# Performance work log

Hardware: AMD Instinct MI355X
Metric: run time of the kernel (lower is better)

Reference implementation:

```python
import jax, jax.numpy as jnp
import numpy as np

N = 100000   # nodes
E = 400000   # edges
P = 250000   # permutations (substructures)
L = 16       # lrp_length
D = 16       # lrp_out_dim
M = P * L    # perm-length rows of the sparse gather matrices


def setup_inputs() -> dict:
    key = jax.random.key(0)
    ks = jax.random.split(key, 16)
    return {
        "nfeat": jax.random.normal(ks[0], (N, D), dtype=jnp.float32),
        "efeat_idx": jax.random.randint(ks[1], (E,), 0, 4, dtype=jnp.int64),
        "n_row": jnp.arange(M, dtype=jnp.int64),
        "n_col": jax.random.randint(ks[2], (M,), 0, N, dtype=jnp.int64),
        "n_val": jax.random.uniform(ks[3], (M,), dtype=jnp.float32),
        "e_row": jnp.arange(M, dtype=jnp.int64),
        "e_col": jax.random.randint(ks[4], (M,), 0, E, dtype=jnp.int64),
        "e_val": jax.random.uniform(ks[5], (M,), dtype=jnp.float32),
        "p_row": jax.random.randint(ks[6], (P,), 0, N, dtype=jnp.int64),
        "p_col": jnp.arange(P, dtype=jnp.int64),
        "p_val": jax.random.uniform(ks[7], (P,), dtype=jnp.float32),
        "degs": jax.random.uniform(ks[8], (N,), dtype=jnp.float32) * 10.0,
        "weights": jax.random.normal(ks[9], (D, D, L), dtype=jnp.float32),
        "bias": jnp.zeros((1, D), dtype=jnp.float32),
        "W0": jax.random.normal(ks[10], (1, 2 * D), dtype=jnp.float32),
        "b0": jnp.zeros((2 * D,), dtype=jnp.float32),
        "W1": jax.random.normal(ks[11], (2 * D, D), dtype=jnp.float32),
        "b1": jnp.zeros((D,), dtype=jnp.float32),
        "bond_emb": jax.random.normal(ks[12], (4, D), dtype=jnp.float32),
    }


def _spmm(row, col, val, mat, m):
    # torch_sparse.spmm(index, value, m, n, mat): out[r] += val * mat[c]
    return jax.ops.segment_sum(val[:, None] * mat[col], row, num_segments=m)


def reference(nfeat, efeat_idx, n_row, n_col, n_val, e_row, e_col, e_val,
              p_row, p_col, p_val, degs, weights, bias, W0, b0, W1, b1, bond_emb):
    efeat = bond_emb[efeat_idx]                              # [E, D]
    x = _spmm(n_row, n_col, n_val, nfeat, M) \
        + _spmm(e_row, e_col, e_val, efeat, M)               # [M, D], M = P*L
    # transpose(0,1).view(D, -1, L).permute(1, 2, 0) -> [P, L, D]
    x = x.T.reshape(D, P, L).transpose(1, 2, 0)
    # einsum('dab,bca->dc'): d=P, a=L, b=D_in, c=D_out
    x = jax.nn.relu(jnp.einsum('pld,dcl->pc', x, weights) + bias)  # [P, D]
    pooled = _spmm(p_row, p_col, p_val, x, N)                # [N, D]
    # degree gate MLP: 1 -> 2D -> D
    fd = jax.nn.relu(degs[:, None] @ W0 + b0) @ W1 + b1      # [N, D]
    return pooled * fd
```

## Files before the change

kernel.cpp:

```cpp
#include <hip/hip_runtime.h>

#define NP 250000
#define NN 100000
#define NE 400000
#define LL 16
#define DD 16
#define MM (NP * LL)
#define NTILES (NP / 16)

typedef __bf16 bf16x8 __attribute__((ext_vector_type(8)));
typedef float f32x4 __attribute__((ext_vector_type(4)));

__device__ __forceinline__ float4 fma4(float a, float4 b, float4 c) {
    float4 r;
    r.x = fmaf(a, b.x, c.x);
    r.y = fmaf(a, b.y, c.y);
    r.z = fmaf(a, b.z, c.z);
    r.w = fmaf(a, b.w, c.w);
    return r;
}

__global__ __launch_bounds__(256) void init_kernel(
    const float* __restrict__ w,
    const float* __restrict__ nfeat,
    const float* __restrict__ bond_emb,
    const int* __restrict__ e_col,
    const int* __restrict__ efeat_idx,
    const float* __restrict__ degs,
    const float* __restrict__ W0,
    const float* __restrict__ b0,
    const float* __restrict__ W1,
    const float* __restrict__ b1,
    __bf16* __restrict__ wfrag,
    __bf16* __restrict__ nfeat_bf,
    __bf16* __restrict__ bond_bf,
    unsigned char* __restrict__ be2,
    float* __restrict__ fd,
    float* __restrict__ out)
{
    int t = blockIdx.x * 256 + threadIdx.x;
    if (t < 4096) {
        int kb = t >> 9;
        int lane = (t >> 3) & 63;
        int j = t & 7;
        int quad = lane >> 4, c = lane & 15;
        int d = ((quad & 1) << 3) + j;
        int l = ((quad >> 1) << 3) + kb;
        wfrag[t] = (__bf16)w[d * 256 + c * 16 + l];
    }
    if (t < NN * DD) {
        nfeat_bf[t] = (__bf16)nfeat[t];
        out[t] = 0.f;
    }
    if (t < 64) bond_bf[t] = (__bf16)bond_emb[t];
    if (t < MM / 4) {
        int4 ec = *(const int4*)(e_col + t * 4);
        unsigned int c0 = (unsigned int)efeat_idx[ec.x] & 3u;
        unsigned int c1 = (unsigned int)efeat_idx[ec.y] & 3u;
        unsigned int c2 = (unsigned int)efeat_idx[ec.z] & 3u;
        unsigned int c3 = (unsigned int)efeat_idx[ec.w] & 3u;
        be2[t] = (unsigned char)(c0 | (c1 << 2) | (c2 << 4) | (c3 << 6));
    }
    if (fd != nullptr && t < NN) {
        float dg = degs[t];
        float4 a0 = ((const float4*)b1)[0];
        float4 a1 = ((const float4*)b1)[1];
        float4 a2 = ((const float4*)b1)[2];
        float4 a3 = ((const float4*)b1)[3];
#pragma unroll
        for (int j2 = 0; j2 < 32; ++j2) {
            float h = fmaxf(fmaf(dg, W0[j2], b0[j2]), 0.f);
            const float4* w1r = (const float4*)(W1 + j2 * 16);
            a0 = fma4(h, w1r[0], a0);
            a1 = fma4(h, w1r[1], a1);
            a2 = fma4(h, w1r[2], a2);
            a3 = fma4(h, w1r[3], a3);
        }
        float4* o = (float4*)(fd + (size_t)t * DD);
        o[0] = a0; o[1] = a1; o[2] = a2; o[3] = a3;
    }
}

__global__ __launch_bounds__(256) void perm_kernel(
    const __bf16* __restrict__ nfeat_bf,
    const int* __restrict__ n_col,
    const float* __restrict__ n_val,
    const float* __restrict__ e_val,
    const unsigned char* __restrict__ be2,
    const int* __restrict__ p_row,
    const float* __restrict__ p_val,
    const __bf16* __restrict__ wfrag,
    const float* __restrict__ bias,
    const __bf16* __restrict__ bond_bf,
    const float* __restrict__ fd,
    float* __restrict__ out)
{
    const int wid = threadIdx.x >> 6;
    const int lane = threadIdx.x & 63;
    const int tile = blockIdx.x * 4 + wid;
    if (tile >= NTILES) return;
    const int quad = lane >> 4;
    const int col = lane & 15;
    const int half = quad & 1;
    const int lhalf = quad >> 1;

    const int pbase = tile * 16;
    const int mbase = (pbase + col) * LL + lhalf * 8;

    int4   nca = *(const int4*)(n_col + mbase);
    int4   ncb = *(const int4*)(n_col + mbase + 4);
    float4 nva = *(const float4*)(n_val + mbase);
    float4 nvb = *(const float4*)(n_val + mbase + 4);
    float4 eva = *(const float4*)(e_val + mbase);
    float4 evb = *(const float4*)(e_val + mbase + 4);
    unsigned int be16 = *(const unsigned short*)(be2 + (mbase >> 2));
    int4   pr  = *(const int4*)(p_row + pbase + quad * 4);
    float4 pvv = *(const float4*)(p_val + pbase + quad * 4);

    int   prs[4] = {pr.x, pr.y, pr.z, pr.w};
    float gv[4] = {1.f, 1.f, 1.f, 1.f};
    if (fd != nullptr) {
#pragma unroll
        for (int r = 0; r < 4; ++r)
            gv[r] = fd[(size_t)prs[r] * DD + col];
    }

    bf16x8 wf[8];
#pragma unroll
    for (int kb = 0; kb < 8; ++kb)
        wf[kb] = *(const bf16x8*)(wfrag + (kb * 64 + lane) * 8);
    const bf16x8 bq0 = *(const bf16x8*)(bond_bf + 0 * 16 + half * 8);
    const bf16x8 bq1 = *(const bf16x8*)(bond_bf + 1 * 16 + half * 8);
    const bf16x8 bq2 = *(const bf16x8*)(bond_bf + 2 * 16 + half * 8);
    const bf16x8 bq3 = *(const bf16x8*)(bond_bf + 3 * 16 + half * 8);
    const float bias_c = bias[col];

    int   ncs[8] = {nca.x, nca.y, nca.z, nca.w, ncb.x, ncb.y, ncb.z, ncb.w};
    float nvs[8] = {nva.x, nva.y, nva.z, nva.w, nvb.x, nvb.y, nvb.z, nvb.w};
    float evs[8] = {eva.x, eva.y, eva.z, eva.w, evb.x, evb.y, evb.z, evb.w};

    bf16x8 nfr[8];
#pragma unroll
    for (int kb = 0; kb < 8; ++kb)
        nfr[kb] = *(const bf16x8*)(nfeat_bf + ncs[kb] * DD + half * 8);

    f32x4 acc = {0.f, 0.f, 0.f, 0.f};
#pragma unroll
    for (int kb = 0; kb < 8; ++kb) {
        unsigned int b = (be16 >> (2 * kb)) & 3u;
        bf16x8 blo = (b & 1) ? bq1 : bq0;
        bf16x8 bhi = (b & 1) ? bq3 : bq2;
        bf16x8 bsel = (b & 2) ? bhi : blo;
        float nv = nvs[kb], ev = evs[kb];
        bf16x8 af;
#pragma unroll
        for (int j = 0; j < 8; ++j)
            af[j] = (__bf16)fmaf(nv, (float)nfr[kb][j], ev * (float)bsel[j]);
        acc = __builtin_amdgcn_mfma_f32_16x16x32_bf16(af, wf[kb], acc, 0, 0, 0);
    }

    float pvs[4] = {pvv.x, pvv.y, pvv.z, pvv.w};
#pragma unroll
    for (int r = 0; r < 4; ++r) {
        float v = fmaxf(acc[r] + bias_c, 0.f) * pvs[r] * gv[r];
        unsafeAtomicAdd(out + (size_t)prs[r] * DD + col, v);
    }
}

__global__ __launch_bounds__(256) void gate_kernel(
    const float* __restrict__ degs,
    const float* __restrict__ W0,
    const float* __restrict__ b0,
    const float* __restrict__ W1,
    const float* __restrict__ b1,
    float* __restrict__ out)
{
    int n = blockIdx.x * 256 + threadIdx.x;
    if (n >= NN) return;
    float dg = degs[n];
    float4 a0 = ((const float4*)b1)[0];
    float4 a1 = ((const float4*)b1)[1];
    float4 a2 = ((const float4*)b1)[2];
    float4 a3 = ((const float4*)b1)[3];
#pragma unroll
    for (int j = 0; j < 32; ++j) {
        float h = fmaxf(fmaf(dg, W0[j], b0[j]), 0.f);
        const float4* w1r = (const float4*)(W1 + j * 16);
        a0 = fma4(h, w1r[0], a0);
        a1 = fma4(h, w1r[1], a1);
        a2 = fma4(h, w1r[2], a2);
        a3 = fma4(h, w1r[3], a3);
    }
    float4* o = (float4*)(out + (size_t)n * DD);
    float4 v0 = o[0], v1 = o[1], v2 = o[2], v3 = o[3];
    v0.x *= a0.x; v0.y *= a0.y; v0.z *= a0.z; v0.w *= a0.w;
    v1.x *= a1.x; v1.y *= a1.y; v1.z *= a1.z; v1.w *= a1.w;
    v2.x *= a2.x; v2.y *= a2.y; v2.z *= a2.z; v2.w *= a2.w;
    v3.x *= a3.x; v3.y *= a3.y; v3.z *= a3.z; v3.w *= a3.w;
    o[0] = v0; o[1] = v1; o[2] = v2; o[3] = v3;
}

extern "C" void kernel_launch(void* const* d_in, const int* in_sizes, int n_in,
                              void* d_out, int out_size, void* d_ws, size_t ws_size,
                              hipStream_t stream) {
    const float* nfeat     = (const float*)d_in[0];
    const int*   efeat_idx = (const int*)d_in[1];
    const int*   n_col     = (const int*)d_in[3];
    const float* n_val     = (const float*)d_in[4];
    const int*   e_col     = (const int*)d_in[6];
    const float* e_val     = (const float*)d_in[7];
    const int*   p_row     = (const int*)d_in[8];
    const float* p_val     = (const float*)d_in[10];
    const float* degs      = (const float*)d_in[11];
    const float* weights   = (const float*)d_in[12];
    const float* bias      = (const float*)d_in[13];
    const float* W0        = (const float*)d_in[14];
    const float* b0        = (const float*)d_in[15];
    const float* W1        = (const float*)d_in[16];
    const float* b1        = (const float*)d_in[17];
    const float* bond_emb  = (const float*)d_in[18];

    float* out = (float*)d_out;

    char* wsb = (char*)d_ws;
    __bf16*        wfrag    = (__bf16*)wsb;
    __bf16*        nfeat_bf = (__bf16*)(wsb + 8192);
    __bf16*        bond_bf  = (__bf16*)(wsb + 8192 + 3200000);
    unsigned char* be2      = (unsigned char*)(wsb + 8192 + 3200000 + 128);
    const size_t base_need  = 8192 + 3200000 + 128 + 1000000;
    const bool   fuse_gate  = ws_size >= base_need + (size_t)NN * DD * 4;
    float*         fd       = fuse_gate ? (float*)(wsb + base_need) : nullptr;

    init_kernel<<<(NN * DD + 255) / 256, 256, 0, stream>>>(
        weights, nfeat, bond_emb, e_col, efeat_idx,
        degs, W0, b0, W1, b1,
        wfrag, nfeat_bf, bond_bf, be2, fd, out);

    perm_kernel<<<(NTILES + 3) / 4, 256, 0, stream>>>(
        nfeat_bf, n_col, n_val, e_val, be2, p_row, p_val,
        wfrag, bias, bond_bf, fd, out);

    if (!fuse_gate)
        gate_kernel<<<(NN + 255) / 256, 256, 0, stream>>>(degs, W0, b0, W1, b1, out);
}
```

Measured before the change: 207.4 us.

## Make perm kernel persistent with double-buffered software-pipelined tile loads

Turns the perm kernel from one wave per tile into a persistent grid of 512 blocks. Each wave strides over tiles with two register buffers, so index loads and the dependent nfeat/fd gathers for upcoming tiles are issued while the MFMA work for the current tile runs. Stream-once inputs use nontemporal loads. The goal is to hide the latency of the dependent gathers. The cost is higher register pressure and fewer resident waves, and the grid may not fill the GPU as well as one block per tile.

```diff
diff --git a/kernel.cpp b/kernel.cpp
--- a/kernel.cpp
+++ b/kernel.cpp
@@ -7,9 +7,12 @@
 #define DD 16
 #define MM (NP * LL)
 #define NTILES (NP / 16)
+#define PERM_BLOCKS 512
+#define GWAVES (PERM_BLOCKS * 4)
 
 typedef __bf16 bf16x8 __attribute__((ext_vector_type(8)));
-typedef float f32x4 __attribute__((ext_vector_type(4)));
+typedef float  f32x4  __attribute__((ext_vector_type(4)));
+typedef int    i32x4  __attribute__((ext_vector_type(4)));
 
 __device__ __forceinline__ float4 fma4(float a, float4 b, float4 c) {
     float4 r;
@@ -81,6 +84,85 @@
     }
 }
 
+
+struct Early { i32x4 nca, ncb, pr; };
+struct Late  { f32x4 nva, nvb, eva, evb, pv; unsigned int be16; };
+struct Gath  { bf16x8 nfr[8]; float gv[4]; int prs[4]; };
+
+__device__ __forceinline__ void load_early(Early& e, int tile, int col, int lhalf, int quad,
+        const int* __restrict__ n_col, const int* __restrict__ p_row) {
+    const int pbase = tile * 16;
+    const int mbase = (pbase + col) * LL + lhalf * 8;
+    e.nca = __builtin_nontemporal_load((const i32x4*)(n_col + mbase));
+    e.ncb = __builtin_nontemporal_load((const i32x4*)(n_col + mbase + 4));
+    e.pr  = __builtin_nontemporal_load((const i32x4*)(p_row + pbase + quad * 4));
+}
+
+__device__ __forceinline__ void load_late(Late& lt, int tile, int col, int lhalf, int quad,
+        const float* __restrict__ n_val, const float* __restrict__ e_val,
+        const unsigned char* __restrict__ be2, const float* __restrict__ p_val) {
+    const int pbase = tile * 16;
+    const int mbase = (pbase + col) * LL + lhalf * 8;
+    lt.nva = __builtin_nontemporal_load((const f32x4*)(n_val + mbase));
+    lt.nvb = __builtin_nontemporal_load((const f32x4*)(n_val + mbase + 4));
+    lt.eva = __builtin_nontemporal_load((const f32x4*)(e_val + mbase));
+    lt.evb = __builtin_nontemporal_load((const f32x4*)(e_val + mbase + 4));
+    lt.pv  = __builtin_nontemporal_load((const f32x4*)(p_val + pbase + quad * 4));
+    lt.be16 = (unsigned int)__builtin_nontemporal_load(
+                  (const unsigned short*)(be2 + (mbase >> 2)));
+}
+
+__device__ __forceinline__ void issue_gathers(Gath& g, const Early& e,
+        const __bf16* __restrict__ nfeat_bf, const float* __restrict__ fd,
+        int half, int col) {
+    int ncs[8] = {e.nca[0], e.nca[1], e.nca[2], e.nca[3],
+                  e.ncb[0], e.ncb[1], e.ncb[2], e.ncb[3]};
+#pragma unroll
+    for (int kb = 0; kb < 8; ++kb)
+        g.nfr[kb] = *(const bf16x8*)(nfeat_bf + (size_t)ncs[kb] * DD + half * 8);
+#pragma unroll
+    for (int r = 0; r < 4; ++r) {
+        g.prs[r] = e.pr[r];
+        g.gv[r] = fd ? fd[(size_t)e.pr[r] * DD + col] : 1.f;
+    }
+}
+
+#define KSTEP(G, KB, NV, EV, J) do { \
+    unsigned int b = (be >> (2 * (KB))) & 3u; \
+    bf16x8 blo = (b & 1) ? bq1 : bq0; \
+    bf16x8 bhi = (b & 1) ? bq3 : bq2; \
+    bf16x8 bsel = (b & 2) ? bhi : blo; \
+    float nv = (NV)[J], ev = (EV)[J]; \
+    bf16x8 af; \
+    _Pragma("unroll") \
+    for (int j = 0; j < 8; ++j) \
+        af[j] = (__bf16)fmaf(nv, (float)G.nfr[KB][j], ev * (float)bsel[j]); \
+    acc = __builtin_amdgcn_mfma_f32_16x16x32_bf16(af, wf[KB], acc, 0, 0, 0); \
+} while (0)
+
+#define STEP(C, N) { \
+    f32x4 acc = {0.f, 0.f, 0.f, 0.f}; \
+    const unsigned int be = lat##C.be16; \
+    KSTEP(g##C, 0, lat##C.nva, lat##C.eva, 0); \
+    KSTEP(g##C, 1, lat##C.nva, lat##C.eva, 1); \
+    KSTEP(g##C, 2, lat##C.nva, lat##C.eva, 2); \
+    KSTEP(g##C, 3, lat##C.nva, lat##C.eva, 3); \
+    if (tn < NTILES) issue_gathers(g##N, ear##N, nfeat_bf, fd, half, col); \
+    if (tf < NTILES) load_early(ear##C, tf, col, lhalf, quad, n_col, p_row); \
+    KSTEP(g##C, 4, lat##C.nvb, lat##C.evb, 0); \
+    KSTEP(g##C, 5, lat##C.nvb, lat##C.evb, 1); \
+    KSTEP(g##C, 6, lat##C.nvb, lat##C.evb, 2); \
+    KSTEP(g##C, 7, lat##C.nvb, lat##C.evb, 3); \
+    _Pragma("unroll") \
+    for (int r = 0; r < 4; ++r) { \
+        float v = fmaxf(acc[r] + bias_c, 0.f) * lat##C.pv[r] * g##C.gv[r]; \
+        unsafeAtomicAdd(out + (size_t)g##C.prs[r] * DD + col, v); \
+    } \
+    if (tf < NTILES) load_late(lat##C, tf, col, lhalf, quad, n_val, e_val, be2, p_val); \
+    if (tn >= NTILES) goto tail_done; \
+    tn = tf; tf += GWAVES; \
+}
+
 __global__ __launch_bounds__(256) void perm_kernel(
     const __bf16* __restrict__ nfeat_bf,
     const int* __restrict__ n_col,
@@ -95,35 +177,13 @@
     const float* __restrict__ fd,
     float* __restrict__ out)
 {
-    const int wid = threadIdx.x >> 6;
+    const int wid  = threadIdx.x >> 6;
     const int lane = threadIdx.x & 63;
-    const int tile = blockIdx.x * 4 + wid;
-    if (tile >= NTILES) return;
+    const int gw   = blockIdx.x * 4 + wid;
     const int quad = lane >> 4;
-    const int col = lane & 15;
+    const int col  = lane & 15;
     const int half = quad & 1;
     const int lhalf = quad >> 1;
-
-    const int pbase = tile * 16;
-    const int mbase = (pbase + col) * LL + lhalf * 8;
-
-    int4   nca = *(const int4*)(n_col + mbase);
-    int4   ncb = *(const int4*)(n_col + mbase + 4);
-    float4 nva = *(const float4*)(n_val + mbase);
-    float4 nvb = *(const float4*)(n_val + mbase + 4);
-    float4 eva = *(const float4*)(e_val + mbase);
-    float4 evb = *(const float4*)(e_val + mbase + 4);
-    unsigned int be16 = *(const unsigned short*)(be2 + (mbase >> 2));
-    int4   pr  = *(const int4*)(p_row + pbase + quad * 4);
-    float4 pvv = *(const float4*)(p_val + pbase + quad * 4);
-
-    int   prs[4] = {pr.x, pr.y, pr.z, pr.w};
-    float gv[4] = {1.f, 1.f, 1.f, 1.f};
-    if (fd != nullptr) {
-#pragma unroll
-        for (int r = 0; r < 4; ++r)
-            gv[r] = fd[(size_t)prs[r] * DD + col];
-    }
 
     bf16x8 wf[8];
 #pragma unroll
@@ -135,36 +195,24 @@
     const bf16x8 bq3 = *(const bf16x8*)(bond_bf + 3 * 16 + half * 8);
     const float bias_c = bias[col];
 
-    int   ncs[8] = {nca.x, nca.y, nca.z, nca.w, ncb.x, ncb.y, ncb.z, ncb.w};
-    float nvs[8] = {nva.x, nva.y, nva.z, nva.w, nvb.x, nvb.y, nvb.z, nvb.w};
-    float evs[8] = {eva.x, eva.y, eva.z, eva.w, evb.x, evb.y, evb.z, evb.w};
-
-    bf16x8 nfr[8];
-#pragma unroll
-    for (int kb = 0; kb < 8; ++kb)
-        nfr[kb] = *(const bf16x8*)(nfeat_bf + ncs[kb] * DD + half * 8);
-
-    f32x4 acc = {0.f, 0.f, 0.f, 0.f};
-#pragma unroll
-    for (int kb = 0; kb < 8; ++kb) {
-        unsigned int b = (be16 >> (2 * kb)) & 3u;
-        bf16x8 blo = (b & 1) ? bq1 : bq0;
-        bf16x8 bhi = (b & 1) ? bq3 : bq2;
-        bf16x8 bsel = (b & 2) ? bhi : blo;
-        float nv = nvs[kb], ev = evs[kb];
-        bf16x8 af;
-#pragma unroll
-        for (int j = 0; j < 8; ++j)
-            af[j] = (__bf16)fmaf(nv, (float)nfr[kb][j], ev * (float)bsel[j]);
-        acc = __builtin_amdgcn_mfma_f32_16x16x32_bf16(af, wf[kb], acc, 0, 0, 0);
-    }
-
-    float pvs[4] = {pvv.x, pvv.y, pvv.z, pvv.w};
-#pragma unroll
-    for (int r = 0; r < 4; ++r) {
-        float v = fmaxf(acc[r] + bias_c, 0.f) * pvs[r] * gv[r];
-        unsafeAtomicAdd(out + (size_t)prs[r] * DD + col, v);
-    }
+    Early earA, earB;
+    Late  latA, latB;
+    Gath  gA, gB;
+
+    int tn = gw + GWAVES;
+    int tf = tn + GWAVES;
+
+    load_early(earA, gw, col, lhalf, quad, n_col, p_row);
+    load_late (latA, gw, col, lhalf, quad, n_val, e_val, be2, p_val);
+    if (tn < NTILES) load_early(earB, tn, col, lhalf, quad, n_col, p_row);
+    issue_gathers(gA, earA, nfeat_bf, fd, half, col);
+    if (tn < NTILES) load_late(latB, tn, col, lhalf, quad, n_val, e_val, be2, p_val);
+
+    for (;;) {
+        STEP(A, B);
+        STEP(B, A);
+    }
+tail_done: ;
 }
 
 __global__ __launch_bounds__(256) void gate_kernel(
@@ -236,7 +284,7 @@
         degs, W0, b0, W1, b1,
         wfrag, nfeat_bf, bond_bf, be2, fd, out);
 
-    perm_kernel<<<(NTILES + 3) / 4, 256, 0, stream>>>(
+    perm_kernel<<<PERM_BLOCKS, 256, 0, stream>>>(
         nfeat_bf, n_col, n_val, e_val, be2, p_row, p_val,
         wfrag, bias, bond_bf, fd, out);
 
```

Result: no change. 204.5 us (-1.4%).
